# Kernel tuning notes

Hardware: AMD Instinct MI355X
Metric: run time of the kernel (lower is better)

The kernel has to match this reference:

```python
import jax, jax.numpy as jnp
import numpy as np

INTERVALS = (1, 2, 4, 8)  # MTGRU update interval per hidden chunk


def _laplacian_hat(adj):
    # PyG ChebConv 'sym' norm, edge_weight=None (binarized), lambda_max=2:
    # L_hat = 2L/lmax - I = -D^-1/2 A D^-1/2 with zero diagonal.
    n = adj.shape[0]
    A = jnp.where(adj != 0, 1.0, 0.0) * (1.0 - jnp.eye(n, dtype=jnp.float32))
    deg = A.sum(axis=1)
    dinv = jnp.where(deg > 0, deg ** -0.5, 0.0)
    return -(dinv[:, None] * A * dinv[None, :])


def _cheb(x, L, W, b):
    # Chebyshev recurrence. x: [..., N, F]; W: [K, F, O]
    Tx0 = x
    out = jnp.einsum('...nf,fo->...no', Tx0, W[0])
    if W.shape[0] > 1:
        Tx1 = jnp.einsum('mn,...nf->...mf', L, x)
        out = out + jnp.einsum('...nf,fo->...no', Tx1, W[1])
        for k in range(2, W.shape[0]):
            Tx2 = 2.0 * jnp.einsum('mn,...nf->...mf', L, Tx1) - Tx0
            out = out + jnp.einsum('...nf,fo->...no', Tx2, W[k])
            Tx0, Tx1 = Tx1, Tx2
    return out + b


def _mtgru(x, h, idx, wi, wh, bi, bh):
    # multi-timescale GRU: hidden chunk k only updates when idx % INTERVALS[k]==0
    hid = h.shape[-1]
    xr, xz, xn = jnp.split(x @ wi + bi, 3, axis=-1)
    hr, hz, hc = jnp.split(h @ wh + bh, 3, axis=-1)
    r = jax.nn.sigmoid(xr + hr)
    z = jax.nn.sigmoid(xz + hz)
    n = jnp.tanh(xn + r * hc)
    h_new = (1.0 - z) * n + z * h
    mask = jnp.repeat((idx % jnp.asarray(INTERVALS)) == 0, hid // len(INTERVALS))
    return jnp.where(mask, h_new, h)


def _fuse(xg, xcg, afc, c2s_w, c2s_b, s2c_w, s2c_b):
    # cross-graph fusion; both updates use the pre-fusion tensors
    xg_new = xg + (jnp.einsum('sc,...cf->...sf', afc, xcg) @ c2s_w + c2s_b)
    xcg_new = xcg + (jnp.einsum('sc,...sf->...cf', afc, xg) @ s2c_w + s2c_b)
    return xg_new, xcg_new


def reference(x_hist, features, c_x_hist, c_features, adj_sta, adj_city, afc_s2c,
              conv_w, conv_b, c_conv_w, c_conv_b,
              gru_wi, gru_wh, gru_bi, gru_bh,
              c_gru_wi, c_gru_wh, c_gru_bi, c_gru_bh,
              fc_w, fc_b, c_fc_w, c_fc_b,
              c2s_w, c2s_b, s2c_w, s2c_b):
    B, T_h, Ns, Dout = x_hist.shape
    Nc = c_x_hist.shape[2]
    H = gru_wh.shape[0]
    L_s = _laplacian_hat(adj_sta)
    L_c = _laplacian_hat(adj_city)

    # ---- history phase: all inputs known ahead, batch GCN + fusion over time ----
    x_all = jnp.moveaxis(jnp.concatenate([x_hist[:, :T_h - 1], features[:, 1:T_h]], -1), 1, 0)   # [Th-1,B,Ns,Din]
    xc_all = jnp.moveaxis(jnp.concatenate([c_x_hist[:, :T_h - 1], c_features[:, 1:T_h]], -1), 1, 0)
    xg = jax.nn.sigmoid(_cheb(x_all, L_s, conv_w, conv_b))
    xcg = jax.nn.sigmoid(_cheb(xc_all, L_c, c_conv_w, c_conv_b))
    xg, xcg = _fuse(xg, xcg, afc_s2c, c2s_w, c2s_b, s2c_w, s2c_b)
    x_gru = jnp.concatenate([x_all, xg], -1)
    xc_gru = jnp.concatenate([xc_all, xcg], -1)

    hn = jnp.zeros((B, Ns, H), jnp.float32)
    hcn = jnp.zeros((B, Nc, H), jnp.float32)

    def hist_step(carry, xs):
        hn, hcn, idx = carry
        xg_t, xcg_t = xs
        hn = _mtgru(xg_t, hn, idx, gru_wi, gru_wh, gru_bi, gru_bh)
        hcn = _mtgru(xcg_t, hcn, idx, c_gru_wi, c_gru_wh, c_gru_bi, c_gru_bh)
        return (hn, hcn, idx + 1), None

    (hn, hcn, idx), _ = jax.lax.scan(hist_step, (hn, hcn, jnp.int32(1)), (x_gru, xc_gru))

    feats_p = jnp.moveaxis(features[:, T_h:], 1, 0)      # [Tp,B,Ns,Dm]
    c_feats_p = jnp.moveaxis(c_features[:, T_h:], 1, 0)

    def pred_step(carry, xs):
        hn, hcn, x_prev, xc_prev, idx = carry
        f, cf = xs
        x = jnp.concatenate([x_prev, f], -1)
        xc = jnp.concatenate([xc_prev, cf], -1)
        xg = jax.nn.sigmoid(_cheb(x, L_s, conv_w, conv_b))
        xcg = jax.nn.sigmoid(_cheb(xc, L_c, c_conv_w, c_conv_b))
        xg, xcg = _fuse(xg, xcg, afc_s2c, c2s_w, c2s_b, s2c_w, s2c_b)
        hn2 = _mtgru(jnp.concatenate([x, xg], -1), hn, idx, gru_wi, gru_wh, gru_bi, gru_bh)
        hcn2 = _mtgru(jnp.concatenate([xc, xcg], -1), hcn, idx, c_gru_wi, c_gru_wh, c_gru_bi, c_gru_bh)
        y = hn2 @ fc_w + fc_b
        yc = hcn2 @ c_fc_w + c_fc_b
        return (hn2, hcn2, y, yc, idx + 1), (y, yc)

    init = (hn, hcn, x_hist[:, T_h - 1], c_x_hist[:, T_h - 1], idx)
    _, (ys, ycs) = jax.lax.scan(pred_step, init, (feats_p, c_feats_p))
    return jnp.moveaxis(ys, 0, 1), jnp.moveaxis(ycs, 0, 1)  # [B,Tp,Ns,1], [B,Tp,Nc,1]


def setup_inputs():
    key = jax.random.key(0)
    ks = jax.random.split(key, 24)
    B, Ns, Nc, T_h, T_p = 8, 4096, 256, 8, 24
    Din, Dout, H, G, K = 28, 1, 64, 64, 2
    Dm, T, Dgru = Din - Dout, T_h + T_p, Din + 64

    def w(k, shape, fan_in):
        return (jax.random.normal(k, shape, jnp.float32) / np.sqrt(fan_in)).astype(jnp.float32)

    return {
        'x_hist': jax.random.normal(ks[0], (B, T_h, Ns, Dout), jnp.float32),
        'features': jax.random.normal(ks[1], (B, T, Ns, Dm), jnp.float32),
        'c_x_hist': jax.random.normal(ks[2], (B, T_h, Nc, Dout), jnp.float32),
        'c_features': jax.random.normal(ks[3], (B, T, Nc, Dm), jnp.float32),
        'adj_sta': (jax.random.uniform(ks[4], (Ns, Ns)) < 0.004).astype(jnp.float32),
        'adj_city': (jax.random.uniform(ks[5], (Nc, Nc)) < 0.1).astype(jnp.float32),
        'afc_s2c': (jax.random.uniform(ks[6], (Ns, Nc)) < (4.0 / Nc)).astype(jnp.float32),
        'conv_w': w(ks[7], (K, Din, G), Din),
        'conv_b': jnp.zeros((G,), jnp.float32),
        'c_conv_w': w(ks[8], (K, Din, G), Din),
        'c_conv_b': jnp.zeros((G,), jnp.float32),
        'gru_wi': w(ks[9], (Dgru, 3 * H), Dgru),
        'gru_wh': w(ks[10], (H, 3 * H), H),
        'gru_bi': jnp.zeros((3 * H,), jnp.float32),
        'gru_bh': jnp.zeros((3 * H,), jnp.float32),
        'c_gru_wi': w(ks[11], (Dgru, 3 * H), Dgru),
        'c_gru_wh': w(ks[12], (H, 3 * H), H),
        'c_gru_bi': jnp.zeros((3 * H,), jnp.float32),
        'c_gru_bh': jnp.zeros((3 * H,), jnp.float32),
        'fc_w': w(ks[13], (H, Dout), H),
        'fc_b': jnp.zeros((Dout,), jnp.float32),
        'c_fc_w': w(ks[14], (H, Dout), H),
        'c_fc_b': jnp.zeros((Dout,), jnp.float32),
        'c2s_w': w(ks[15], (G, G), G),
        'c2s_b': jnp.zeros((G,), jnp.float32),
        's2c_w': w(ks[16], (G, G), G),
        's2c_b': jnp.zeros((G,), jnp.float32),
    }
```

## Files before the change

kernel.cpp:

```cpp
#include <hip/hip_runtime.h>
#include <math.h>

typedef short bf16x8 __attribute__((ext_vector_type(8)));
typedef float f32x4 __attribute__((ext_vector_type(4)));

#define B 8
#define NS 4096
#define NC 256
#define TH 8
#define TP 24
#define T_ALL 32
#define DIN 28
#define DM 27
#define G 64
#define H 64
#define NG3 192
#define NSTEP 31

#define NTHR 256
#define NBLK_B 1024
#define SROWS 32
#define CROWS 2
#define NBLK_A 2048
#define AS 16
#define AR 17

#define XCW 224
#define KIT 7
#define NT 16
#define WFRAG (KIT*NT*64*8)
#define CVFRAG (2*4*64*8)

#define WS_ELL 64
#define WF_ELL 32
#define WFT_ELL 128

struct Params {
  const float *x_hist, *feat_s, *c_x_hist, *feat_c, *adj_s, *adj_c, *afc;
  const float *conv_w, *conv_b, *c_conv_w, *c_conv_b;
  const float *gru_wi, *gru_wh, *gru_bi, *gru_bh;
  const float *c_gru_wi, *c_gru_wh, *c_gru_bi, *c_gru_bh;
  const float *fc_w, *fc_b, *c_fc_w, *c_fc_b;
  const float *c2s_w, *c2s_b, *s2c_w, *s2c_b;
  int *deg_s, *ellc_s; float *ellv_s, *dinv_s;
  int *deg_c, *ellc_c; float *ellv_c, *dinv_c;
  int *degf, *ellf;
  int *degfT, *ellfT;
  float *xg_s, *xg_c, *xp_s, *xp_c;
  unsigned short *xsh, *xsl;
  unsigned short *xch, *xcl;
  unsigned short *wSh, *wSl, *wCh, *wCl;
  unsigned short *wcvSh, *wcvSl, *wcvCh, *wcvCl;
  float *aA_s, *aA_c;
  float *out;
};

__device__ __forceinline__ float sigm_(float x) { return 1.0f / (1.0f + expf(-x)); }

__device__ __forceinline__ unsigned short bf16rn(float f) {
  unsigned u = __float_as_uint(f);
  u += 0x7fffu + ((u >> 16) & 1u);
  return (unsigned short)(u >> 16);
}
__device__ __forceinline__ float bf16tof(unsigned short h) {
  return __uint_as_float(((unsigned)h) << 16);
}
__device__ __forceinline__ void split1(float f, unsigned short& hi, unsigned short& lo) {
  hi = bf16rn(f);
  lo = bf16rn(f - bf16tof(hi));
}

__device__ __forceinline__ int sidx(int i, int c) {
  return i * 64 + (c ^ ((i & 7) << 3));
}

__device__ float wcat_val(int k, int c, const float* wi, const float* wh,
                          const float* bi, const float* bh) {
  if (k < 92)  { return (c < 192) ? wi[k * NG3 + c] : 0.0f; }
  if (k < 156) {
    int kk = k - 92;
    if (c < 128) return wh[kk * NG3 + c];
    if (c < 192) return 0.0f;
    return wh[kk * NG3 + (c - 64)];
  }
  if (k == 156) {
    if (c < 128) return bi[c] + bh[c];
    if (c < 192) return bi[c];
    return bh[c - 64];
  }
  return 0.0f;
}

__device__ float wcat2_val(int k, int c, const float* wi, const float* wh,
                           const float* bi, const float* bh,
                           const float* wm, const float* bm) {
  if (k < 92) return wcat_val(k, c, wi, wh, bi, bh);
  if (k < 156) {
    int f = k - 92;
    float s = 0.0f;
    for (int g = 0; g < G; g++)
      s += wm[f * G + g] * wcat_val(28 + g, c, wi, wh, bi, bh);
    return s;
  }
  if (k < 220) return wcat_val(92 + (k - 156), c, wi, wh, bi, bh);
  if (k == 220) {
    float s = wcat_val(156, c, wi, wh, bi, bh);
    for (int g = 0; g < G; g++)
      s += bm[g] * wcat_val(28 + g, c, wi, wh, bi, bh);
    return s;
  }
  return 0.0f;
}

__device__ __forceinline__ float xval(const Params& p, int sta, int hist, int step,
                                      int b, int n, int f) {
  if (f == 0) {
    if (hist) return sta ? p.x_hist[((size_t)b * TH + step) * NS + n]
                         : p.c_x_hist[((size_t)b * TH + step) * NC + n];
    return sta ? p.xp_s[b * NS + n] : p.xp_c[b * NC + n];
  }
  int tf = step + 1;
  return sta ? p.feat_s[(((size_t)b * T_ALL + tf) * NS + n) * DM + (f - 1)]
             : p.feat_c[(((size_t)b * T_ALL + tf) * NC + n) * DM + (f - 1)];
}

__device__ void build_tables(const Params& p, int bid, int tid, int nblk) {
  const int lane = tid & 63;
  const int gw = bid * 4 + (tid >> 6);
  const int nw = nblk * 4;

  for (int r = gw; r < NS; r += nw) {
    int base = 0;
    for (int n0 = 0; n0 < NS; n0 += 64) {
      int n = n0 + lane;
      float v = p.adj_s[(size_t)r * NS + n];
      bool fl = (v != 0.0f) && (n != r);
      unsigned long long m = __ballot(fl);
      if (fl) {
        int pos = base + (int)__popcll(m & ((1ull << lane) - 1ull));
        if (pos < WS_ELL) p.ellc_s[r * WS_ELL + pos] = n;
      }
      base += (int)__popcll(m);
    }
    int deg = base < WS_ELL ? base : WS_ELL;
    for (int s = deg + lane; s < WS_ELL; s += 64) p.ellc_s[r * WS_ELL + s] = 0;
    if (lane == 0) {
      p.deg_s[r] = deg;
      p.dinv_s[r] = base > 0 ? 1.0f / sqrtf((float)base) : 0.0f;
    }
  }
  for (int r = gw; r < NS; r += nw) {
    int base = 0;
    for (int n0 = 0; n0 < NC; n0 += 64) {
      int n = n0 + lane;
      bool fl = p.afc[(size_t)r * NC + n] != 0.0f;
      unsigned long long m = __ballot(fl);
      if (fl) {
        int pos = base + (int)__popcll(m & ((1ull << lane) - 1ull));
        if (pos < WF_ELL) p.ellf[r * WF_ELL + pos] = n;
      }
      base += (int)__popcll(m);
    }
    int deg = base < WF_ELL ? base : WF_ELL;
    for (int s = deg + lane; s < WF_ELL; s += 64) p.ellf[r * WF_ELL + s] = 0;
    if (lane == 0) p.degf[r] = deg;
  }
  for (int r = gw; r < NC; r += nw) {
    int base = 0;
    for (int n0 = 0; n0 < NC; n0 += 64) {
      int n = n0 + lane;
      float v = p.adj_c[(size_t)r * NC + n];
      bool fl = (v != 0.0f) && (n != r);
      unsigned long long m = __ballot(fl);
      if (fl) {
        int pos = base + (int)__popcll(m & ((1ull << lane) - 1ull));
        if (pos < WS_ELL) p.ellc_c[r * WS_ELL + pos] = n;
      }
      base += (int)__popcll(m);
    }
    int deg = base < WS_ELL ? base : WS_ELL;
    for (int s = deg + lane; s < WS_ELL; s += 64) p.ellc_c[r * WS_ELL + s] = 0;
    if (lane == 0) {
      p.deg_c[r] = deg;
      p.dinv_c[r] = base > 0 ? 1.0f / sqrtf((float)base) : 0.0f;
    }
  }
  for (int r = gw; r < NC; r += nw) {
    int base = 0;
    for (int n0 = 0; n0 < NS; n0 += 64) {
      int n = n0 + lane;
      bool fl = p.afc[(size_t)n * NC + r] != 0.0f;
      unsigned long long m = __ballot(fl);
      if (fl) {
        int pos = base + (int)__popcll(m & ((1ull << lane) - 1ull));
        if (pos < WFT_ELL) p.ellfT[r * WFT_ELL + pos] = n;
      }
      base += (int)__popcll(m);
    }
    int deg = base < WFT_ELL ? base : WFT_ELL;
    for (int s = deg + lane; s < WFT_ELL; s += 64) p.ellfT[r * WFT_ELL + s] = 0;
    if (lane == 0) p.degfT[r] = deg;
  }

  const int gid = bid * NTHR + tid, ntot = nblk * NTHR;
  for (int i = gid; i < B * NS; i += ntot)
    p.xp_s[i] = p.x_hist[((size_t)(i / NS) * TH + (TH - 1)) * NS + (i % NS)];
  for (int i = gid; i < B * NC; i += ntot)
    p.xp_c[i] = p.c_x_hist[((size_t)(i / NC) * TH + (TH - 1)) * NC + (i % NC)];

  for (int u = gid; u < WFRAG; u += ntot) {
    int j = u & 7, l = (u >> 3) & 63, t = (u >> 9) & 15, q = u >> 13;
    int k = q * 32 + ((l >> 4) << 3) + j;
    int c = t * 16 + (l & 15);
    float ws = wcat2_val(k, c, p.gru_wi, p.gru_wh, p.gru_bi, p.gru_bh, p.c2s_w, p.c2s_b);
    unsigned short hh, ll;
    split1(ws, hh, ll);
    p.wSh[u] = hh; p.wSl[u] = ll;
    float wc = wcat2_val(k, c, p.c_gru_wi, p.c_gru_wh, p.c_gru_bi, p.c_gru_bh, p.s2c_w, p.s2c_b);
    split1(wc, hh, ll);
    p.wCh[u] = hh; p.wCl[u] = ll;
  }
  for (int u = gid; u < CVFRAG; u += ntot) {
    int j = u & 7, l = (u >> 3) & 63, t = (u >> 9) & 3, q = u >> 11;
    int k = q * 32 + ((l >> 4) << 3) + j;
    int c = t * 16 + (l & 15);
    float vs = (k < 56) ? p.conv_w[k * G + c] : 0.0f;
    unsigned short hh, ll;
    split1(vs, hh, ll);
    p.wcvSh[u] = hh; p.wcvSl[u] = ll;
    float vc = (k < 56) ? p.c_conv_w[k * G + c] : 0.0f;
    split1(vc, hh, ll);
    p.wcvCh[u] = hh; p.wcvCl[u] = ll;
  }
  for (int u = gid; u < B * NS * XCW; u += ntot) {
    p.xsh[u] = ((u % XCW) == 220) ? 0x3F80 : 0;
    p.xsl[u] = 0;
  }
  for (int u = gid; u < B * NC * XCW; u += ntot) {
    p.xch[u] = ((u % XCW) == 220) ? 0x3F80 : 0;
    p.xcl[u] = 0;
  }
}

__device__ void ellv_fill(const Params& p, int gid, int ntot) {
  for (int s = gid; s < NS * WS_ELL; s += ntot) {
    int r = s >> 6, k = s & (WS_ELL - 1);
    p.ellv_s[s] = (k < p.deg_s[r]) ? -p.dinv_s[r] * p.dinv_s[p.ellc_s[s]] : 0.0f;
  }
  for (int s = gid; s < NC * WS_ELL; s += ntot) {
    int r = s >> 6, k = s & (WS_ELL - 1);
    p.ellv_c[s] = (k < p.deg_c[r]) ? -p.dinv_c[r] * p.dinv_c[p.ellc_c[s]] : 0.0f;
  }
}

__global__ __launch_bounds__(NTHR) void precompA2_kernel(Params p) {
  __shared__ unsigned short lh[AR * 64];
  __shared__ unsigned short llo[AR * 64];
  const int bid = blockIdx.x & 2047;
  const int step = blockIdx.x >> 11;
  const int hist = (step < TH - 1) ? 1 : 0;
  const int tid = threadIdx.x;
  const int b = bid >> 8;

  for (int u = tid; u < AR * 8; u += NTHR) {
    lh[sidx(u >> 3, 56 + (u & 7))] = 0;
    llo[sidx(u >> 3, 56 + (u & 7))] = 0;
  }

  for (int q = tid; q < AR * DIN; q += NTHR) {
    int i = q / DIN, f = q % DIN;
    int sta = (i < AS);
    int n;
    const int* cc; const float* vv; int trip;
    if (sta) {
      n = (bid * AS + i) & 4095;
      cc = &p.ellc_s[n * WS_ELL]; vv = &p.ellv_s[n * WS_ELL];
      trip = (p.deg_s[n] + 7) & ~7;
    } else {
      n = bid & 255;
      cc = &p.ellc_c[n * WS_ELL]; vv = &p.ellv_c[n * WS_ELL];
      trip = (p.deg_c[n] + 7) & ~7;
    }
    float xv = 0.0f, acc = 0.0f;
    if (f == 0) {
      if (hist) {
        const float* bh = sta ? (p.x_hist + ((size_t)b * TH + step) * NS)
                              : (p.c_x_hist + ((size_t)b * TH + step) * NC);
        xv = bh[n];
        for (int e = 0; e < trip; e += 8) {
          float xv8[8];
#pragma unroll
          for (int u = 0; u < 8; u++) xv8[u] = bh[cc[e + u]];
#pragma unroll
          for (int u = 0; u < 8; u++) acc += vv[e + u] * xv8[u];
        }
      }
    } else {
      const float* bf = sta
        ? (p.feat_s + ((size_t)(b * T_ALL + step + 1) * NS) * DM + (f - 1))
        : (p.feat_c + ((size_t)(b * T_ALL + step + 1) * NC) * DM + (f - 1));
      xv = bf[(size_t)n * DM];
      for (int e = 0; e < trip; e += 8) {
        float xv8[8];
#pragma unroll
        for (int u = 0; u < 8; u++) xv8[u] = bf[(size_t)cc[e + u] * DM];
#pragma unroll
        for (int u = 0; u < 8; u++) acc += vv[e + u] * xv8[u];
      }
    }
    unsigned short hh, ll;
    split1(xv, hh, ll);
    lh[sidx(i, f)] = hh; llo[sidx(i, f)] = ll;
    split1(acc, hh, ll);
    lh[sidx(i, 28 + f)] = hh; llo[sidx(i, 28 + f)] = ll;
  }
  __syncthreads();

  const int l = tid & 63;
  const int wv = tid >> 6;
  f32x4 a1; f32x4 a2;
  a1[0] = 0.f; a1[1] = 0.f; a1[2] = 0.f; a1[3] = 0.f;
  a2[0] = 0.f; a2[1] = 0.f; a2[2] = 0.f; a2[3] = 0.f;
  const bf16x8* WVSh = (const bf16x8*)p.wcvSh;
  const bf16x8* WVSl = (const bf16x8*)p.wcvSl;
  const bf16x8* WVCh = (const bf16x8*)p.wcvCh;
  const bf16x8* WVCl = (const bf16x8*)p.wcvCl;
#pragma unroll
  for (int q = 0; q < 2; q++) {
    int kc = q * 32 + ((l >> 4) << 3);
    bf16x8 xh = *(const bf16x8*)&lh[sidx(l & 15, kc)];
    bf16x8 xl = *(const bf16x8*)&llo[sidx(l & 15, kc)];
    bf16x8 ch_, cl_;
    if ((l & 15) == 0) {
      ch_ = *(const bf16x8*)&lh[sidx(AS, kc)];
      cl_ = *(const bf16x8*)&llo[sidx(AS, kc)];
    } else {
#pragma unroll
      for (int j = 0; j < 8; j++) { ch_[j] = 0; cl_[j] = 0; }
    }
    int u = (q * 4 + wv) * 64 + l;
    bf16x8 bh_ = WVSh[u];
    bf16x8 bl_ = WVSl[u];
    a1 = __builtin_amdgcn_mfma_f32_16x16x32_bf16(xh, bh_, a1, 0, 0, 0);
    a1 = __builtin_amdgcn_mfma_f32_16x16x32_bf16(xl, bh_, a1, 0, 0, 0);
    a1 = __builtin_amdgcn_mfma_f32_16x16x32_bf16(xh, bl_, a1, 0, 0, 0);
    bf16x8 gh_ = WVCh[u];
    bf16x8 gl_ = WVCl[u];
    a2 = __builtin_amdgcn_mfma_f32_16x16x32_bf16(ch_, gh_, a2, 0, 0, 0);
    a2 = __builtin_amdgcn_mfma_f32_16x16x32_bf16(cl_, gh_, a2, 0, 0, 0);
    a2 = __builtin_amdgcn_mfma_f32_16x16x32_bf16(ch_, gl_, a2, 0, 0, 0);
  }

  const int g = wv * 16 + (l & 15);
  float* dst_s = p.aA_s + (size_t)step * (B * NS * G);
  float* dst_c = p.aA_c + (size_t)step * (B * NC * G);
  float bias = p.conv_b[g];
#pragma unroll
  for (int r = 0; r < 4; r++) {
    int row = ((l >> 4) << 2) + r;
    float v = a1[r] + bias;
    if (hist) v = sigm_(v);
    dst_s[(size_t)(bid * AS + row) * G + g] = v;
  }
  if ((l >> 4) == 0) {
    float v = a2[0] + p.c_conv_b[g];
    if (hist) v = sigm_(v);
    dst_c[(size_t)bid * G + g] = v;
  }
}

__global__ __launch_bounds__(NTHR) void stepA_lite_kernel(Params p, int step, int hist) {
  const int tid = threadIdx.x;
  const int l = tid & 63, wv = tid >> 6;
  const int wid = blockIdx.x * 4 + wv;
  if (wid < B * NS) {
    const int smn = wid, b = smn >> 12, n = smn & 4095;
    float x0 = hist ? p.x_hist[((size_t)b * TH + step) * NS + n] : p.xp_s[smn];
    float xg;
    const float* aA = p.aA_s + (size_t)step * (B * NS * G) + (size_t)smn * G;
    if (hist) {
      xg = aA[l];
    } else {
      float v = p.ellv_s[n * WS_ELL + l];
      int c = p.ellc_s[n * WS_ELL + l];
      float t = v * p.xp_s[b * NS + c];
#pragma unroll
      for (int m = 32; m; m >>= 1) t += __shfl_xor(t, m, 64);
      float acc = aA[l] + x0 * p.conv_w[l] + t * p.conv_w[DIN * G + l];
      xg = sigm_(acc);
      p.xg_s[(size_t)smn * G + l] = xg;
    }
    unsigned short hh, ll;
    split1(xg, hh, ll);
    size_t o = (size_t)smn * XCW;
    p.xsh[o + 28 + l] = hh; p.xsl[o + 28 + l] = ll;
    if (l < DIN) {
      float xv = (l == 0) ? x0
        : p.feat_s[(((size_t)b * T_ALL + step + 1) * NS + n) * DM + (l - 1)];
      split1(xv, hh, ll);
      p.xsh[o + l] = hh; p.xsl[o + l] = ll;
    }
  } else if (wid < B * NS + B * NC) {
    const int cm = wid - B * NS, b = cm >> 8, n = cm & 255;
    float x0 = hist ? p.c_x_hist[((size_t)b * TH + step) * NC + n] : p.xp_c[cm];
    float xg;
    const float* aA = p.aA_c + (size_t)step * (B * NC * G) + (size_t)cm * G;
    if (hist) {
      xg = aA[l];
    } else {
      float v = p.ellv_c[n * WS_ELL + l];
      int c = p.ellc_c[n * WS_ELL + l];
      float t = v * p.xp_c[b * NC + c];
#pragma unroll
      for (int m = 32; m; m >>= 1) t += __shfl_xor(t, m, 64);
      float acc = aA[l] + x0 * p.c_conv_w[l] + t * p.c_conv_w[DIN * G + l];
      xg = sigm_(acc);
      p.xg_c[(size_t)cm * G + l] = xg;
    }
    unsigned short hh, ll;
    split1(xg, hh, ll);
    size_t o = (size_t)cm * XCW;
    p.xch[o + 28 + l] = hh; p.xcl[o + 28 + l] = ll;
    if (l < DIN) {
      float xv = (l == 0) ? x0
        : p.feat_c[(((size_t)b * T_ALL + step + 1) * NC + n) * DM + (l - 1)];
      split1(xv, hh, ll);
      p.xch[o + l] = hh; p.xcl[o + l] = ll;
    }
  }
}

__global__ __launch_bounds__(NTHR) void stepA_kernel(Params p, int step, int hist) {
  __shared__ float xa[AR][DIN];
  __shared__ float lx[AR][DIN];
  const int bid = blockIdx.x, tid = threadIdx.x;
  for (int q = tid; q < AR * DIN; q += NTHR) {
    int i = q / DIN, f = q % DIN;
    int sta = (i < AS);
    int b, n;
    const int* cc; const float* vv; int trip;
    if (sta) {
      int smn = bid * AS + i; b = smn >> 12; n = smn & 4095;
      cc = &p.ellc_s[n * WS_ELL]; vv = &p.ellv_s[n * WS_ELL];
      trip = (p.deg_s[n] + 7) & ~7;
    } else {
      b = bid >> 8; n = bid & 255;
      cc = &p.ellc_c[n * WS_ELL]; vv = &p.ellv_c[n * WS_ELL];
      trip = (p.deg_c[n] + 7) & ~7;
    }
    float xv = xval(p, sta, hist, step, b, n, f);
    xa[i][f] = xv;
    unsigned short hh, ll;
    split1(xv, hh, ll);
    if (sta) {
      size_t o = (size_t)(bid * AS + i) * XCW + f;
      p.xsh[o] = hh; p.xsl[o] = ll;
    } else {
      size_t o = (size_t)bid * XCW + f;
      p.xch[o] = hh; p.xcl[o] = ll;
    }
    float acc = 0.0f;
    for (int e = 0; e < trip; e += 8) {
      float xv8[8];
#pragma unroll
      for (int u = 0; u < 8; u++) xv8[u] = xval(p, sta, hist, step, b, cc[e + u], f);
#pragma unroll
      for (int u = 0; u < 8; u++) acc += vv[e + u] * xv8[u];
    }
    lx[i][f] = acc;
  }
  __syncthreads();
  for (int q = tid; q < AR * G; q += NTHR) {
    int i = q >> 6, g = q & 63;
    int sta = (i < AS);
    const float* W = sta ? p.conv_w : p.c_conv_w;
    float acc = (sta ? p.conv_b : p.c_conv_b)[g];
#pragma unroll 4
    for (int f = 0; f < DIN; f++)
      acc += xa[i][f] * W[f * G + g] + lx[i][f] * W[DIN * G + f * G + g];
    float s = sigm_(acc);
    unsigned short hh, ll;
    split1(s, hh, ll);
    if (sta) {
      p.xg_s[(size_t)(bid * AS + i) * G + g] = s;
      size_t o = (size_t)(bid * AS + i) * XCW + 28 + g;
      p.xsh[o] = hh; p.xsl[o] = ll;
    } else {
      p.xg_c[(size_t)bid * G + g] = s;
      size_t o = (size_t)bid * XCW + 28 + g;
      p.xch[o] = hh; p.xcl[o] = ll;
    }
  }
}

__global__ __launch_bounds__(NTHR, 4) void stepB_kernel(Params p, int step, int hist, int idx) {
  __shared__ float cityfc[4][CROWS];
  __shared__ float fcs[4][SROWS];
  const int bid = blockIdx.x, tid = threadIdx.x;
  unsigned short* xsh = p.xsh + (size_t)bid * SROWS * XCW;
  unsigned short* xsl = p.xsl + (size_t)bid * SROWS * XCW;
  unsigned short* xch = p.xch + (size_t)bid * CROWS * XCW;
  unsigned short* xcl = p.xcl + (size_t)bid * CROWS * XCW;

#pragma unroll
  for (int k = 0; k < (SROWS * G) / NTHR; k++) {
    int q = tid + k * NTHR;
    int i = q >> 6, g = q & 63;
    int smn = bid * SROWS + i; int b = smn >> 12; int r = smn & 4095;
    int dg = p.degf[r];
    const int* cc = &p.ellf[r * WF_ELL];
    size_t bb = (size_t)b * NC;
    float acc = 0.0f;
    int e = 0;
    for (; e + 4 <= dg; e += 4) {
      acc += p.xg_c[(bb + cc[e]) * G + g] + p.xg_c[(bb + cc[e + 1]) * G + g]
           + p.xg_c[(bb + cc[e + 2]) * G + g] + p.xg_c[(bb + cc[e + 3]) * G + g];
    }
    for (; e < dg; e++) acc += p.xg_c[(bb + cc[e]) * G + g];
    unsigned short hh, ll;
    split1(acc, hh, ll);
    xsh[(size_t)i * XCW + 92 + g] = hh;
    xsl[(size_t)i * XCW + 92 + g] = ll;
  }
  {
    int g = (tid >> 2) & 63;
    int quar = tid & 3;
#pragma unroll
    for (int ci = 0; ci < CROWS; ci++) {
      int cm = bid * CROWS + ci; int b = cm >> 8; int r = cm & 255;
      int dg = p.degfT[r];
      const int* cc = &p.ellfT[r * WFT_ELL];
      int dq = (dg + 3) >> 2;
      int e0 = quar * dq;
      int e1 = e0 + dq; if (e1 > dg) e1 = dg; if (e0 > dg) e0 = dg;
      size_t bb = (size_t)b * NS;
      float acc = 0.0f;
      int e = e0;
      for (; e + 4 <= e1; e += 4) {
        acc += p.xg_s[(bb + cc[e]) * G + g] + p.xg_s[(bb + cc[e + 1]) * G + g]
             + p.xg_s[(bb + cc[e + 2]) * G + g] + p.xg_s[(bb + cc[e + 3]) * G + g];
      }
      for (; e < e1; e++) acc += p.xg_s[(bb + cc[e]) * G + g];
      acc += __shfl_down(acc, 2, 4);
      acc += __shfl_down(acc, 1, 4);
      if (quar == 0) {
        unsigned short hh, ll;
        split1(acc, hh, ll);
        xch[(size_t)ci * XCW + 92 + g] = hh;
        xcl[(size_t)ci * XCW + 92 + g] = ll;
      }
    }
  }
  __syncthreads();

  const int l = tid & 63;
  const int wv = tid >> 6;
  f32x4 accS[8];
  f32x4 accC[4];
#pragma unroll
  for (int t = 0; t < 8; t++) { accS[t][0] = 0.f; accS[t][1] = 0.f; accS[t][2] = 0.f; accS[t][3] = 0.f; }
#pragma unroll
  for (int t = 0; t < 4; t++) { accC[t][0] = 0.f; accC[t][1] = 0.f; accC[t][2] = 0.f; accC[t][3] = 0.f; }
  const bf16x8* WSh = (const bf16x8*)p.wSh;
  const bf16x8* WSl = (const bf16x8*)p.wSl;
  const bf16x8* WCh = (const bf16x8*)p.wCh;
  const bf16x8* WCl = (const bf16x8*)p.wCl;

#pragma unroll
  for (int q = 0; q < KIT; q++) {
    int kc = q * 32 + ((l >> 4) << 3);
    bf16x8 aS0h = *(const bf16x8*)(xsh + (size_t)(l & 15) * XCW + kc);
    bf16x8 aS0l = *(const bf16x8*)(xsl + (size_t)(l & 15) * XCW + kc);
    bf16x8 aS1h = *(const bf16x8*)(xsh + (size_t)(16 + (l & 15)) * XCW + kc);
    bf16x8 aS1l = *(const bf16x8*)(xsl + (size_t)(16 + (l & 15)) * XCW + kc);
    bf16x8 aCh, aCl;
    if ((l & 15) < CROWS) {
      aCh = *(const bf16x8*)(xch + (size_t)(l & 15) * XCW + kc);
      aCl = *(const bf16x8*)(xcl + (size_t)(l & 15) * XCW + kc);
    } else {
#pragma unroll
      for (int j = 0; j < 8; j++) { aCh[j] = 0; aCl[j] = 0; }
    }
    int base = q * (NT * 64) + l;
#pragma unroll
    for (int tt = 0; tt < 4; tt++) {
      if (tt == 2 && q == 5) continue;
      if (tt == 3 && q < 4) continue;
      int toff = base + (wv + tt * 4) * 64;
      bf16x8 wh_ = WSh[toff];
      bf16x8 wl_ = WSl[toff];
      accS[tt]     = __builtin_amdgcn_mfma_f32_16x16x32_bf16(aS0h, wh_, accS[tt], 0, 0, 0);
      accS[tt]     = __builtin_amdgcn_mfma_f32_16x16x32_bf16(aS0l, wh_, accS[tt], 0, 0, 0);
      accS[tt]     = __builtin_amdgcn_mfma_f32_16x16x32_bf16(aS0h, wl_, accS[tt], 0, 0, 0);
      accS[4 + tt] = __builtin_amdgcn_mfma_f32_16x16x32_bf16(aS1h, wh_, accS[4 + tt], 0, 0, 0);
      accS[4 + tt] = __builtin_amdgcn_mfma_f32_16x16x32_bf16(aS1l, wh_, accS[4 + tt], 0, 0, 0);
      accS[4 + tt] = __builtin_amdgcn_mfma_f32_16x16x32_bf16(aS1h, wl_, accS[4 + tt], 0, 0, 0);
      bf16x8 ch_ = WCh[toff];
      bf16x8 cl_ = WCl[toff];
      accC[tt] = __builtin_amdgcn_mfma_f32_16x16x32_bf16(aCh, ch_, accC[tt], 0, 0, 0);
      accC[tt] = __builtin_amdgcn_mfma_f32_16x16x32_bf16(aCl, ch_, accC[tt], 0, 0, 0);
      accC[tt] = __builtin_amdgcn_mfma_f32_16x16x32_bf16(aCh, cl_, accC[tt], 0, 0, 0);
    }
  }
  __syncthreads();

  const int pred = !hist;
  const int t_out = step - (TH - 1);
  const int j = wv * 16 + (l & 15);
  const int upd = ((idx & ((1 << wv) - 1)) == 0);
  float fcacc[8];
  {
    float fwj = p.fc_w[j];
#pragma unroll
    for (int rt = 0; rt < 2; rt++) {
#pragma unroll
      for (int r = 0; r < 4; r++) {
        int row = rt * 16 + ((l >> 4) << 2) + r;
        float rr = sigm_(accS[rt * 4 + 0][r]);
        float zz = sigm_(accS[rt * 4 + 1][r]);
        float nn = tanhf(accS[rt * 4 + 2][r] + rr * accS[rt * 4 + 3][r]);
        size_t o = (size_t)row * XCW + 156 + j;
        float ho = bf16tof(xsh[o]) + bf16tof(xsl[o]);
        float hn = upd ? ((1.0f - zz) * nn + zz * ho) : ho;
        unsigned short hh, ll;
        split1(hn, hh, ll);
        xsh[o] = hh; xsl[o] = ll;
        fcacc[rt * 4 + r] = fwj * hn;
      }
    }
  }
  float cfc[CROWS] = {0.f, 0.f};
  if ((l >> 4) == 0) {
    float fwj = p.c_fc_w[j];
#pragma unroll
    for (int r = 0; r < CROWS; r++) {
      float rr = sigm_(accC[0][r]);
      float zz = sigm_(accC[1][r]);
      float nn = tanhf(accC[2][r] + rr * accC[3][r]);
      size_t o = (size_t)r * XCW + 156 + j;
      float ho = bf16tof(xch[o]) + bf16tof(xcl[o]);
      float hn = upd ? ((1.0f - zz) * nn + zz * ho) : ho;
      unsigned short hh, ll;
      split1(hn, hh, ll);
      xch[o] = hh; xcl[o] = ll;
      cfc[r] = fwj * hn;
    }
  }
  if (pred) {
#pragma unroll
    for (int rt = 0; rt < 2; rt++) {
#pragma unroll
      for (int r = 0; r < 4; r++) {
        float v = fcacc[rt * 4 + r];
        v += __shfl_down(v, 8, 16);
        v += __shfl_down(v, 4, 16);
        v += __shfl_down(v, 2, 16);
        v += __shfl_down(v, 1, 16);
        if ((l & 15) == 0) fcs[wv][rt * 16 + ((l >> 4) << 2) + r] = v;
      }
    }
#pragma unroll
    for (int r = 0; r < CROWS; r++) {
      float v = cfc[r];
      v += __shfl_down(v, 8, 16);
      v += __shfl_down(v, 4, 16);
      v += __shfl_down(v, 2, 16);
      v += __shfl_down(v, 1, 16);
      if (l == 0) cityfc[wv][r] = v;
    }
    __syncthreads();
    if (tid < SROWS) {
      float y = fcs[0][tid] + fcs[1][tid] + fcs[2][tid] + fcs[3][tid] + p.fc_b[0];
      int smn = bid * SROWS + tid; int b = smn >> 12; int n = smn & 4095;
      p.out[((size_t)b * TP + t_out) * NS + n] = y;
      p.xp_s[smn] = y;
    }
    if (tid >= 64 && tid < 64 + CROWS) {
      int r = tid - 64;
      float y = cityfc[0][r] + cityfc[1][r] + cityfc[2][r] + cityfc[3][r] + p.c_fc_b[0];
      int cm = bid * CROWS + r; int b = cm >> 8; int n = cm & 255;
      p.out[(size_t)B * TP * NS + ((size_t)b * TP + t_out) * NC + n] = y;
      p.xp_c[cm] = y;
    }
  }
}

__global__ __launch_bounds__(NTHR) void build_kernel(Params p) {
  build_tables(p, blockIdx.x, threadIdx.x, gridDim.x);
}
__global__ __launch_bounds__(NTHR) void ellv_kernel(Params p) {
  ellv_fill(p, blockIdx.x * NTHR + threadIdx.x, gridDim.x * NTHR);
}

extern "C" void kernel_launch(void* const* d_in, const int* in_sizes, int n_in,
                              void* d_out, int out_size, void* d_ws, size_t ws_size,
                              hipStream_t stream) {
  Params p;
  p.x_hist   = (const float*)d_in[0];
  p.feat_s   = (const float*)d_in[1];
  p.c_x_hist = (const float*)d_in[2];
  p.feat_c   = (const float*)d_in[3];
  p.adj_s    = (const float*)d_in[4];
  p.adj_c    = (const float*)d_in[5];
  p.afc      = (const float*)d_in[6];
  p.conv_w   = (const float*)d_in[7];
  p.conv_b   = (const float*)d_in[8];
  p.c_conv_w = (const float*)d_in[9];
  p.c_conv_b = (const float*)d_in[10];
  p.gru_wi   = (const float*)d_in[11];
  p.gru_wh   = (const float*)d_in[12];
  p.gru_bi   = (const float*)d_in[13];
  p.gru_bh   = (const float*)d_in[14];
  p.c_gru_wi = (const float*)d_in[15];
  p.c_gru_wh = (const float*)d_in[16];
  p.c_gru_bi = (const float*)d_in[17];
  p.c_gru_bh = (const float*)d_in[18];
  p.fc_w     = (const float*)d_in[19];
  p.fc_b     = (const float*)d_in[20];
  p.c_fc_w   = (const float*)d_in[21];
  p.c_fc_b   = (const float*)d_in[22];
  p.c2s_w    = (const float*)d_in[23];
  p.c2s_b    = (const float*)d_in[24];
  p.s2c_w    = (const float*)d_in[25];
  p.s2c_b    = (const float*)d_in[26];

  char* wp = (char*)d_ws;
  auto alloc = [&](size_t bytes) -> char* {
    char* q = wp;
    wp += (bytes + 255) & ~(size_t)255;
    return q;
  };
  p.deg_s  = (int*)alloc(NS * 4);
  p.dinv_s = (float*)alloc(NS * 4);
  p.ellc_s = (int*)alloc((size_t)NS * WS_ELL * 4);
  p.ellv_s = (float*)alloc((size_t)NS * WS_ELL * 4);
  p.deg_c  = (int*)alloc(NC * 4);
  p.dinv_c = (float*)alloc(NC * 4);
  p.ellc_c = (int*)alloc((size_t)NC * WS_ELL * 4);
  p.ellv_c = (float*)alloc((size_t)NC * WS_ELL * 4);
  p.degf   = (int*)alloc(NS * 4);
  p.ellf   = (int*)alloc((size_t)NS * WF_ELL * 4);
  p.degfT  = (int*)alloc(NC * 4);
  p.ellfT  = (int*)alloc((size_t)NC * WFT_ELL * 4);
  p.xg_s   = (float*)alloc((size_t)B * NS * G * 4);
  p.xg_c   = (float*)alloc((size_t)B * NC * G * 4);
  p.xp_s   = (float*)alloc((size_t)B * NS * 4);
  p.xp_c   = (float*)alloc((size_t)B * NC * 4);
  p.xsh    = (unsigned short*)alloc((size_t)B * NS * XCW * 2);
  p.xsl    = (unsigned short*)alloc((size_t)B * NS * XCW * 2);
  p.xch    = (unsigned short*)alloc((size_t)B * NC * XCW * 2);
  p.xcl    = (unsigned short*)alloc((size_t)B * NC * XCW * 2);
  p.wSh    = (unsigned short*)alloc((size_t)WFRAG * 2);
  p.wSl    = (unsigned short*)alloc((size_t)WFRAG * 2);
  p.wCh    = (unsigned short*)alloc((size_t)WFRAG * 2);
  p.wCl    = (unsigned short*)alloc((size_t)WFRAG * 2);
  p.wcvSh  = (unsigned short*)alloc((size_t)CVFRAG * 2);
  p.wcvSl  = (unsigned short*)alloc((size_t)CVFRAG * 2);
  p.wcvCh  = (unsigned short*)alloc((size_t)CVFRAG * 2);
  p.wcvCl  = (unsigned short*)alloc((size_t)CVFRAG * 2);
  p.aA_s   = (float*)alloc((size_t)NSTEP * B * NS * G * 4);
  p.aA_c   = (float*)alloc((size_t)NSTEP * B * NC * G * 4);
  p.out    = (float*)d_out;

  const bool big = ((size_t)(wp - (char*)d_ws) <= ws_size);

  build_kernel<<<2048, NTHR, 0, stream>>>(p);
  ellv_kernel<<<2048, NTHR, 0, stream>>>(p);
  if (big) {
    precompA2_kernel<<<NSTEP * 2048, NTHR, 0, stream>>>(p);
    for (int step = 0; step < NSTEP; step++) {
      int hist = (step < TH - 1) ? 1 : 0;
      stepA_lite_kernel<<<(B * NS + B * NC) / 4, NTHR, 0, stream>>>(p, step, hist);
      Params pb = p;
      if (hist) {
        pb.xg_s = p.aA_s + (size_t)step * (B * NS * G);
        pb.xg_c = p.aA_c + (size_t)step * (B * NC * G);
      }
      stepB_kernel<<<NBLK_B, NTHR, 0, stream>>>(pb, step, hist, step + 1);
    }
  } else {
    for (int step = 0; step < NSTEP; step++) {
      int hist = (step < TH - 1) ? 1 : 0;
      stepA_kernel<<<NBLK_A, NTHR, 0, stream>>>(p, step, hist);
      stepB_kernel<<<NBLK_B, NTHR, 0, stream>>>(p, step, hist, step + 1);
    }
  }
}
```

Measured before the change: 2.892 ms.

## Double stepB block size to cut padded city-GRU MFMA work

stepB now runs 512-thread blocks covering 64 station rows and 4 city rows, with half as many blocks. Two groups of four waves each take 32 station rows, and only the first group runs the city GRU MFMAs. Each 16-row city tile now holds 4 valid rows instead of 2, which halves the redundant padded city MFMA and weight loads, and per-block launch overhead also drops. The trade-off is that launch_bounds(512,4) asks for twice the resident waves per CU, which tightens the register budget and risks spills given the large accumulator set.

```diff
diff --git a/kernel.cpp b/kernel.cpp
--- a/kernel.cpp
+++ b/kernel.cpp
@@ -18,9 +18,10 @@
 #define NSTEP 31
 
 #define NTHR 256
-#define NBLK_B 1024
-#define SROWS 32
-#define CROWS 2
+#define NBLK_B 512
+#define NTHR_B 512
+#define BROWS 64
+#define BCROWS 4
 #define NBLK_A 2048
 #define AS 16
 #define AR 17
@@ -493,20 +494,20 @@
   }
 }
 
-__global__ __launch_bounds__(NTHR, 4) void stepB_kernel(Params p, int step, int hist, int idx) {
-  __shared__ float cityfc[4][CROWS];
-  __shared__ float fcs[4][SROWS];
+__global__ __launch_bounds__(NTHR_B, 4) void stepB_kernel(Params p, int step, int hist, int idx) {
+  __shared__ float cityfc[4][BCROWS];
+  __shared__ float fcs[4][BROWS];
   const int bid = blockIdx.x, tid = threadIdx.x;
-  unsigned short* xsh = p.xsh + (size_t)bid * SROWS * XCW;
-  unsigned short* xsl = p.xsl + (size_t)bid * SROWS * XCW;
-  unsigned short* xch = p.xch + (size_t)bid * CROWS * XCW;
-  unsigned short* xcl = p.xcl + (size_t)bid * CROWS * XCW;
-
-#pragma unroll
-  for (int k = 0; k < (SROWS * G) / NTHR; k++) {
-    int q = tid + k * NTHR;
+  unsigned short* xsh = p.xsh + (size_t)bid * BROWS * XCW;
+  unsigned short* xsl = p.xsl + (size_t)bid * BROWS * XCW;
+  unsigned short* xch = p.xch + (size_t)bid * BCROWS * XCW;
+  unsigned short* xcl = p.xcl + (size_t)bid * BCROWS * XCW;
+
+#pragma unroll
+  for (int k = 0; k < (BROWS * G) / NTHR_B; k++) {
+    int q = tid + k * NTHR_B;
     int i = q >> 6, g = q & 63;
-    int smn = bid * SROWS + i; int b = smn >> 12; int r = smn & 4095;
+    int smn = bid * BROWS + i; int b = smn >> 12; int r = smn & 4095;
     int dg = p.degf[r];
     const int* cc = &p.ellf[r * WF_ELL];
     size_t bb = (size_t)b * NC;
@@ -523,11 +524,14 @@
     xsl[(size_t)i * XCW + 92 + g] = ll;
   }
   {
-    int g = (tid >> 2) & 63;
-    int quar = tid & 3;
-#pragma unroll
-    for (int ci = 0; ci < CROWS; ci++) {
-      int cm = bid * CROWS + ci; int b = cm >> 8; int r = cm & 255;
+    int half = tid >> 8;
+    int t256 = tid & 255;
+    int g = (t256 >> 2) & 63;
+    int quar = t256 & 3;
+#pragma unroll
+    for (int c2 = 0; c2 < 2; c2++) {
+      int ci = half * 2 + c2;
+      int cm = bid * BCROWS + ci; int b = cm >> 8; int r = cm & 255;
       int dg = p.degfT[r];
       const int* cc = &p.ellfT[r * WFT_ELL];
       int dq = (dg + 3) >> 2;
@@ -555,6 +559,9 @@
 
   const int l = tid & 63;
   const int wv = tid >> 6;
+  const int quad = wv >> 2;
+  const int wq = wv & 3;
+  const int rowbase = quad * 32;
   f32x4 accS[8];
   f32x4 accC[4];
 #pragma unroll
@@ -569,12 +576,12 @@
 #pragma unroll
   for (int q = 0; q < KIT; q++) {
     int kc = q * 32 + ((l >> 4) << 3);
-    bf16x8 aS0h = *(const bf16x8*)(xsh + (size_t)(l & 15) * XCW + kc);
-    bf16x8 aS0l = *(const bf16x8*)(xsl + (size_t)(l & 15) * XCW + kc);
-    bf16x8 aS1h = *(const bf16x8*)(xsh + (size_t)(16 + (l & 15)) * XCW + kc);
-    bf16x8 aS1l = *(const bf16x8*)(xsl + (size_t)(16 + (l & 15)) * XCW + kc);
+    bf16x8 aS0h = *(const bf16x8*)(xsh + (size_t)(rowbase + (l & 15)) * XCW + kc);
+    bf16x8 aS0l = *(const bf16x8*)(xsl + (size_t)(rowbase + (l & 15)) * XCW + kc);
+    bf16x8 aS1h = *(const bf16x8*)(xsh + (size_t)(rowbase + 16 + (l & 15)) * XCW + kc);
+    bf16x8 aS1l = *(const bf16x8*)(xsl + (size_t)(rowbase + 16 + (l & 15)) * XCW + kc);
     bf16x8 aCh, aCl;
-    if ((l & 15) < CROWS) {
+    if (quad == 0 && (l & 15) < BCROWS) {
       aCh = *(const bf16x8*)(xch + (size_t)(l & 15) * XCW + kc);
       aCl = *(const bf16x8*)(xcl + (size_t)(l & 15) * XCW + kc);
     } else {
@@ -586,7 +593,7 @@
     for (int tt = 0; tt < 4; tt++) {
       if (tt == 2 && q == 5) continue;
       if (tt == 3 && q < 4) continue;
-      int toff = base + (wv + tt * 4) * 64;
+      int toff = base + (wq + tt * 4) * 64;
       bf16x8 wh_ = WSh[toff];
       bf16x8 wl_ = WSl[toff];
       accS[tt]     = __builtin_amdgcn_mfma_f32_16x16x32_bf16(aS0h, wh_, accS[tt], 0, 0, 0);
@@ -595,19 +602,21 @@
       accS[4 + tt] = __builtin_amdgcn_mfma_f32_16x16x32_bf16(aS1h, wh_, accS[4 + tt], 0, 0, 0);
       accS[4 + tt] = __builtin_amdgcn_mfma_f32_16x16x32_bf16(aS1l, wh_, accS[4 + tt], 0, 0, 0);
       accS[4 + tt] = __builtin_amdgcn_mfma_f32_16x16x32_bf16(aS1h, wl_, accS[4 + tt], 0, 0, 0);
-      bf16x8 ch_ = WCh[toff];
-      bf16x8 cl_ = WCl[toff];
-      accC[tt] = __builtin_amdgcn_mfma_f32_16x16x32_bf16(aCh, ch_, accC[tt], 0, 0, 0);
-      accC[tt] = __builtin_amdgcn_mfma_f32_16x16x32_bf16(aCl, ch_, accC[tt], 0, 0, 0);
-      accC[tt] = __builtin_amdgcn_mfma_f32_16x16x32_bf16(aCh, cl_, accC[tt], 0, 0, 0);
+      if (quad == 0) {
+        bf16x8 ch_ = WCh[toff];
+        bf16x8 cl_ = WCl[toff];
+        accC[tt] = __builtin_amdgcn_mfma_f32_16x16x32_bf16(aCh, ch_, accC[tt], 0, 0, 0);
+        accC[tt] = __builtin_amdgcn_mfma_f32_16x16x32_bf16(aCl, ch_, accC[tt], 0, 0, 0);
+        accC[tt] = __builtin_amdgcn_mfma_f32_16x16x32_bf16(aCh, cl_, accC[tt], 0, 0, 0);
+      }
     }
   }
   __syncthreads();
 
   const int pred = !hist;
   const int t_out = step - (TH - 1);
-  const int j = wv * 16 + (l & 15);
-  const int upd = ((idx & ((1 << wv) - 1)) == 0);
+  const int j = wq * 16 + (l & 15);
+  const int upd = ((idx & ((1 << wq) - 1)) == 0);
   float fcacc[8];
   {
     float fwj = p.fc_w[j];
@@ -615,7 +624,7 @@
     for (int rt = 0; rt < 2; rt++) {
 #pragma unroll
       for (int r = 0; r < 4; r++) {
-        int row = rt * 16 + ((l >> 4) << 2) + r;
+        int row = rowbase + rt * 16 + ((l >> 4) << 2) + r;
         float rr = sigm_(accS[rt * 4 + 0][r]);
         float zz = sigm_(accS[rt * 4 + 1][r]);
         float nn = tanhf(accS[rt * 4 + 2][r] + rr * accS[rt * 4 + 3][r]);
@@ -629,11 +638,11 @@
       }
     }
   }
-  float cfc[CROWS] = {0.f, 0.f};
-  if ((l >> 4) == 0) {
+  float cfc[BCROWS] = {0.f, 0.f, 0.f, 0.f};
+  if (quad == 0 && (l >> 4) == 0) {
     float fwj = p.c_fc_w[j];
 #pragma unroll
-    for (int r = 0; r < CROWS; r++) {
+    for (int r = 0; r < BCROWS; r++) {
       float rr = sigm_(accC[0][r]);
       float zz = sigm_(accC[1][r]);
       float nn = tanhf(accC[2][r] + rr * accC[3][r]);
@@ -656,29 +665,31 @@
         v += __shfl_down(v, 4, 16);
         v += __shfl_down(v, 2, 16);
         v += __shfl_down(v, 1, 16);
-        if ((l & 15) == 0) fcs[wv][rt * 16 + ((l >> 4) << 2) + r] = v;
-      }
-    }
-#pragma unroll
-    for (int r = 0; r < CROWS; r++) {
-      float v = cfc[r];
-      v += __shfl_down(v, 8, 16);
-      v += __shfl_down(v, 4, 16);
-      v += __shfl_down(v, 2, 16);
-      v += __shfl_down(v, 1, 16);
-      if (l == 0) cityfc[wv][r] = v;
+        if ((l & 15) == 0) fcs[wq][rowbase + rt * 16 + ((l >> 4) << 2) + r] = v;
+      }
+    }
+    if (quad == 0) {
+#pragma unroll
+      for (int r = 0; r < BCROWS; r++) {
+        float v = cfc[r];
+        v += __shfl_down(v, 8, 16);
+        v += __shfl_down(v, 4, 16);
+        v += __shfl_down(v, 2, 16);
+        v += __shfl_down(v, 1, 16);
+        if (l == 0) cityfc[wq][r] = v;
+      }
     }
     __syncthreads();
-    if (tid < SROWS) {
+    if (tid < BROWS) {
       float y = fcs[0][tid] + fcs[1][tid] + fcs[2][tid] + fcs[3][tid] + p.fc_b[0];
-      int smn = bid * SROWS + tid; int b = smn >> 12; int n = smn & 4095;
+      int smn = bid * BROWS + tid; int b = smn >> 12; int n = smn & 4095;
       p.out[((size_t)b * TP + t_out) * NS + n] = y;
       p.xp_s[smn] = y;
     }
-    if (tid >= 64 && tid < 64 + CROWS) {
+    if (tid >= 64 && tid < 64 + BCROWS) {
       int r = tid - 64;
       float y = cityfc[0][r] + cityfc[1][r] + cityfc[2][r] + cityfc[3][r] + p.c_fc_b[0];
-      int cm = bid * CROWS + r; int b = cm >> 8; int n = cm & 255;
+      int cm = bid * BCROWS + r; int b = cm >> 8; int n = cm & 255;
       p.out[(size_t)B * TP * NS + ((size_t)b * TP + t_out) * NC + n] = y;
       p.xp_c[cm] = y;
     }
@@ -776,13 +787,13 @@
         pb.xg_s = p.aA_s + (size_t)step * (B * NS * G);
         pb.xg_c = p.aA_c + (size_t)step * (B * NC * G);
       }
-      stepB_kernel<<<NBLK_B, NTHR, 0, stream>>>(pb, step, hist, step + 1);
+      stepB_kernel<<<NBLK_B, NTHR_B, 0, stream>>>(pb, step, hist, step + 1);
     }
   } else {
     for (int step = 0; step < NSTEP; step++) {
       int hist = (step < TH - 1) ? 1 : 0;
       stepA_kernel<<<NBLK_A, NTHR, 0, stream>>>(p, step, hist);
-      stepB_kernel<<<NBLK_B, NTHR, 0, stream>>>(p, step, hist, step + 1);
-    }
-  }
-}
+      stepB_kernel<<<NBLK_B, NTHR_B, 0, stream>>>(p, step, hist, step + 1);
+    }
+  }
+}
```

Result: faster. 2.797 ms (-3.3%).
